# Kernel optimization log

Measured on AMD Instinct MI355X. Metric: run time of the kernel, lower is better.

Reference implementation:

```python
import jax, jax.numpy as jnp
import numpy as np

H, W = 200, 200            # image_size
X_RANGE = (0.0, 100.0)
Y_RANGE = (0.0, 100.0)
SIZE = 36                   # kernel 'size' from source
SIGMA = 3.0
K = SIZE + 1                # kernel is 37x37 (arange(-18, 19))


def _gaussian_kernel():
    r = jnp.arange(-(SIZE // 2), SIZE // 2 + 1, dtype=jnp.float32)
    k1 = jnp.exp(-(r ** 2) / (2.0 * SIGMA ** 2))
    k2 = k1[:, None] * k1[None, :]
    return k2 / k2.sum()    # [K, K]


def setup_inputs() -> dict:
    key = jax.random.key(0)
    # trajectory coords in world units [0, 100) -> spread over whole map
    x_t = jax.random.uniform(key, (512, 64, 2), dtype=jnp.float32) * 100.0
    return {"x_t": x_t}


def reference(x_t):
    B, T, _ = x_t.shape
    x_scale = W / (X_RANGE[1] - X_RANGE[0])
    y_scale = H / (Y_RANGE[1] - Y_RANGE[0])
    # .long() in torch truncates toward zero; inputs are >= 0 here so astype(int32) matches
    x_pix = ((x_t[:, :, 0] - X_RANGE[0]) * x_scale).astype(jnp.int32)   # [B, T]
    y_pix = H - ((x_t[:, :, 1] - Y_RANGE[0]) * y_scale).astype(jnp.int32)
    valid = ~(jnp.isnan(x_t[:, :, 0]) | jnp.isnan(x_t[:, :, 1]))        # [B, T]

    half = SIZE // 2
    x_start = jnp.clip(x_pix - half, 0, W - SIZE)
    y_start = jnp.clip(y_pix - half, 0, H - SIZE)
    x_end = jnp.clip(x_pix + half, 0, W)
    y_end = jnp.clip(y_pix + half, 0, H)
    kx = x_end - x_start    # patch width  (<= 36, kernel[:,:kx] = top-left slice)
    ky = y_end - y_start    # patch height

    kern = _gaussian_kernel()                       # [K, K]
    r = jnp.arange(K)
    c = jnp.arange(K)
    # mask: kernel[:ky, :kx] slice, and point validity            [B, T, K, K]
    mask = ((r[None, None, :, None] < ky[..., None, None])
            & (c[None, None, None, :] < kx[..., None, None])
            & valid[..., None, None])
    vals = jnp.where(mask, kern[None, None, :, :], 0.0)            # [B, T, K, K]
    rows = jnp.clip(y_start[..., None, None] + r[None, None, :, None], 0, H - 1)
    cols = jnp.clip(x_start[..., None, None] + c[None, None, None, :], 0, W - 1)
    rows = jnp.broadcast_to(rows, (B, T, K, K))
    cols = jnp.broadcast_to(cols, (B, T, K, K))
    flat = (rows * W + cols).reshape(B, -1)                        # [B, T*K*K]

    # parallel scatter-add splat of all Gaussian patches
    heat = jnp.zeros((B, H * W), jnp.float32)
    heat = heat.at[jnp.arange(B)[:, None], flat].add(vals.reshape(B, -1))
    heat = heat.reshape(B, H, W)

    # per-image max normalization (max over dim1 then dim2 == max over both)
    m = heat.max(axis=(1, 2), keepdims=True)
    return heat / (m + 1e-10)
```

## Files before the change

### kernel.cpp

```cpp
#include <hip/hip_runtime.h>


#define NT 64
#define TDIM 224
#define BLK 512

typedef short bf16x8 __attribute__((ext_vector_type(8)));
typedef float f32x4  __attribute__((ext_vector_type(4)));

static __device__ inline unsigned short f2bf(float f) {
    unsigned int u = __float_as_uint(f);
    u = (u + 0x7FFFu + ((u >> 16) & 1u)) >> 16;
    return (unsigned short)u;
}

struct __align__(16) SMem {
    unsigned short M[TDIM][64];
    unsigned short stg[8][16][200];
    float k1f[37];
    float wmax[8];
};

__global__ __launch_bounds__(BLK, 4) void heatmap_kernel(const float* __restrict__ x_t,
                                                         float* __restrict__ out) {
    __shared__ SMem s;
    const int tid  = threadIdx.x;
    const int lane = tid & 63;
    const int wv   = tid >> 6;
    const int b    = blockIdx.x;
    const int swl  = (lane & 7) << 4;

    {
        uint4 z = {0u, 0u, 0u, 0u};
        uint4* base = (uint4*)s.M;
        #pragma unroll
        for (int i = 0; i < 4; ++i) {
            const int idx = tid + BLK * i;
            if (idx < 1792) base[idx] = z;
        }
    }
    if (tid < 37) {
        float sum = 0.0f, mine = 0.0f;
        #pragma unroll
        for (int i = 0; i < 37; ++i) {
            float r = (float)(i - 18);
            float v = expf(-(r * r) * (1.0f / 18.0f));
            sum += v;
            if (i == tid) mine = v;
        }
        s.k1f[tid] = mine / sum;
    }
    __syncthreads();

    const int p = tid >> 3, j = tid & 7;
    const float2 xy = *(const float2*)(x_t + (size_t)b * 128 + 2 * p);
    const bool valid = (xy.x == xy.x) && (xy.y == xy.y);
    const int xp = (int)(xy.x * 2.0f);
    const int yp = 200 - (int)(xy.y * 2.0f);
    const int xs = min(max(xp - 18, 0), 164);
    const int ys = min(max(yp - 18, 0), 164);
    const int kx = valid ? (min(max(xp + 18, 0), 200) - xs) : 0;
    const int ky = valid ? (min(max(yp + 18, 0), 200) - ys) : 0;

    #pragma unroll
    for (int i = 0; i < 5; ++i) {
        const int rel = j * 5 + i;
        if (rel < ky) {
            const int row = ys + rel;
            *(unsigned short*)((char*)s.M + row * 128 + ((2 * p) ^ ((row & 7) << 4)))
                = f2bf(s.k1f[rel]);
        }
    }
    __syncthreads();

    const int s1 = wv, s2 = wv + 8;
    bf16x8 A10, A11, A20, A21;
    {
        const char* ab = (const char*)s.M + (16 * s1 + (lane & 15)) * 128;
        A10 = *(const bf16x8*)(ab + ((16 * (lane >> 4)) ^ swl));
        A11 = *(const bf16x8*)(ab + ((16 * (lane >> 4) + 64) ^ swl));
    }
    if (s2 < 13) {
        const char* ab = (const char*)s.M + (16 * s2 + (lane & 15)) * 128;
        A20 = *(const bf16x8*)(ab + ((16 * (lane >> 4)) ^ swl));
        A21 = *(const bf16x8*)(ab + ((16 * (lane >> 4) + 64) ^ swl));
    } else { A20 = A10; A21 = A11; }
    __syncthreads();

    {
        uint4 z = {0u, 0u, 0u, 0u};
        uint4* base = (uint4*)s.M;
        #pragma unroll
        for (int i = 0; i < 4; ++i) {
            const int idx = tid + BLK * i;
            if (idx < 1792) base[idx] = z;
        }
    }
    __syncthreads();
    #pragma unroll
    for (int i = 0; i < 5; ++i) {
        const int rel = j * 5 + i;
        if (rel < kx) {
            const int row = xs + rel;
            *(unsigned short*)((char*)s.M + row * 128 + ((2 * p) ^ ((row & 7) << 4)))
                = f2bf(s.k1f[rel]);
        }
    }
    __syncthreads();

    auto compute_strip = [&](bf16x8 A0, bf16x8 A1, f32x4* acc) {
        #pragma unroll
        for (int t = 0; t < 13; ++t) {
            acc[t][0] = 0.0f; acc[t][1] = 0.0f; acc[t][2] = 0.0f; acc[t][3] = 0.0f;
        }
        #pragma unroll
        for (int t = 0; t < 13; ++t) {
            const char* bb = (const char*)s.M + (16 * t + (lane & 15)) * 128;
            bf16x8 B0 = *(const bf16x8*)(bb + ((16 * (lane >> 4)) ^ swl));
            bf16x8 B1 = *(const bf16x8*)(bb + ((16 * (lane >> 4) + 64) ^ swl));
            acc[t] = __builtin_amdgcn_mfma_f32_16x16x32_bf16(A0, B0, acc[t], 0, 0, 0);
            acc[t] = __builtin_amdgcn_mfma_f32_16x16x32_bf16(A1, B1, acc[t], 0, 0, 0);
        }
    };

    float gmax = 0.0f;
    {
        f32x4 acc[13];
        compute_strip(A10, A11, acc);
        #pragma unroll
        for (int t = 0; t < 13; ++t)
            #pragma unroll
            for (int r = 0; r < 4; ++r) gmax = fmaxf(gmax, acc[t][r]);
        if (s2 < 13) {
            compute_strip(A20, A21, acc);
            #pragma unroll
            for (int t = 0; t < 13; ++t)
                #pragma unroll
                for (int r = 0; r < 4; ++r) gmax = fmaxf(gmax, acc[t][r]);
        }
    }
    #pragma unroll
    for (int off = 32; off > 0; off >>= 1) gmax = fmaxf(gmax, __shfl_xor(gmax, off));
    if (lane == 0) s.wmax[wv] = gmax;
    __syncthreads();
    float mm = s.wmax[0];
    #pragma unroll
    for (int w = 1; w < 8; ++w) mm = fmaxf(mm, s.wmax[w]);
    const float scale = 1.0f / (mm + 1e-10f);

    float* ob = out + (size_t)b * (200 * 200);
    unsigned short* st = &s.stg[wv][0][0];
    auto do_strip = [&](int ss, bf16x8 A0, bf16x8 A1) {
        f32x4 acc[13];
        compute_strip(A0, A1, acc);
        const int r0l = 4 * (lane >> 4), c0l = lane & 15;
        #pragma unroll
        for (int t = 0; t < 13; ++t) {
            const int col = 16 * t + c0l;
            if (col < 200) {
                #pragma unroll
                for (int r = 0; r < 4; ++r)
                    st[(r0l + r) * 200 + col] = f2bf(acc[t][r] * scale);
            }
        }
        __threadfence_block();
        const int nrow = min(16, 200 - 16 * ss);
        float* obs = ob + (size_t)(16 * ss) * 200;
        for (int i = lane; i < nrow * 50; i += 64) {
            uint2 v = *(const uint2*)(st + 4 * i);
            float4 o;
            o.x = __uint_as_float(v.x << 16);
            o.y = __uint_as_float(v.x & 0xFFFF0000u);
            o.z = __uint_as_float(v.y << 16);
            o.w = __uint_as_float(v.y & 0xFFFF0000u);
            *(float4*)(obs + 4 * i) = o;
        }
    };
    do_strip(s1, A10, A11);
    if (s2 < 13) do_strip(s2, A20, A21);
}

extern "C" void kernel_launch(void* const* d_in, const int* in_sizes, int n_in,
                              void* d_out, int out_size, void* d_ws, size_t ws_size,
                              hipStream_t stream) {
    const float* x_t = (const float*)d_in[0];
    float* out = (float*)d_out;
    const int B = in_sizes[0] / (NT * 2);
    heatmap_kernel<<<B, BLK, 0, stream>>>(x_t, out);
}
```

Before: 23.33 us.

## Stage unnormalized MFMA results once and process two images per block

Instead of computing the separable Gaussian outer-product via MFMA twice (once for the max, once for output), each wave stores unnormalized bf16 results into a doubled LDS staging buffer and applies the normalization scale during the global write. Each block now processes two images sequentially, halving the grid, and the occupancy hint in launch bounds is removed. This removes redundant matrix work but increases LDS usage, which reduces blocks per CU, and reduces parallelism across the grid.

```diff
diff --git a/kernel.cpp b/kernel.cpp
--- a/kernel.cpp
+++ b/kernel.cpp
@@ -16,29 +16,19 @@
 
 struct __align__(16) SMem {
     unsigned short M[TDIM][64];
-    unsigned short stg[8][16][200];
+    unsigned short stg[8][2][16][200];
     float k1f[37];
     float wmax[8];
 };
 
-__global__ __launch_bounds__(BLK, 4) void heatmap_kernel(const float* __restrict__ x_t,
-                                                         float* __restrict__ out) {
+__global__ __launch_bounds__(BLK) void heatmap_kernel(const float* __restrict__ x_t,
+                                                      float* __restrict__ out) {
     __shared__ SMem s;
     const int tid  = threadIdx.x;
     const int lane = tid & 63;
     const int wv   = tid >> 6;
-    const int b    = blockIdx.x;
     const int swl  = (lane & 7) << 4;
 
-    {
-        uint4 z = {0u, 0u, 0u, 0u};
-        uint4* base = (uint4*)s.M;
-        #pragma unroll
-        for (int i = 0; i < 4; ++i) {
-            const int idx = tid + BLK * i;
-            if (idx < 1792) base[idx] = z;
-        }
-    }
     if (tid < 37) {
         float sum = 0.0f, mine = 0.0f;
         #pragma unroll
@@ -50,134 +40,138 @@
         }
         s.k1f[tid] = mine / sum;
     }
-    __syncthreads();
-
-    const int p = tid >> 3, j = tid & 7;
-    const float2 xy = *(const float2*)(x_t + (size_t)b * 128 + 2 * p);
-    const bool valid = (xy.x == xy.x) && (xy.y == xy.y);
-    const int xp = (int)(xy.x * 2.0f);
-    const int yp = 200 - (int)(xy.y * 2.0f);
-    const int xs = min(max(xp - 18, 0), 164);
-    const int ys = min(max(yp - 18, 0), 164);
-    const int kx = valid ? (min(max(xp + 18, 0), 200) - xs) : 0;
-    const int ky = valid ? (min(max(yp + 18, 0), 200) - ys) : 0;
-
-    #pragma unroll
-    for (int i = 0; i < 5; ++i) {
-        const int rel = j * 5 + i;
-        if (rel < ky) {
-            const int row = ys + rel;
-            *(unsigned short*)((char*)s.M + row * 128 + ((2 * p) ^ ((row & 7) << 4)))
-                = f2bf(s.k1f[rel]);
-        }
-    }
-    __syncthreads();
 
     const int s1 = wv, s2 = wv + 8;
-    bf16x8 A10, A11, A20, A21;
-    {
-        const char* ab = (const char*)s.M + (16 * s1 + (lane & 15)) * 128;
-        A10 = *(const bf16x8*)(ab + ((16 * (lane >> 4)) ^ swl));
-        A11 = *(const bf16x8*)(ab + ((16 * (lane >> 4) + 64) ^ swl));
-    }
-    if (s2 < 13) {
-        const char* ab = (const char*)s.M + (16 * s2 + (lane & 15)) * 128;
-        A20 = *(const bf16x8*)(ab + ((16 * (lane >> 4)) ^ swl));
-        A21 = *(const bf16x8*)(ab + ((16 * (lane >> 4) + 64) ^ swl));
-    } else { A20 = A10; A21 = A11; }
-    __syncthreads();
 
-    {
-        uint4 z = {0u, 0u, 0u, 0u};
-        uint4* base = (uint4*)s.M;
+    for (int img = 0; img < 2; ++img) {
+        const int b = 2 * blockIdx.x + img;
+
+        __syncthreads();
+        {
+            uint4 z = {0u, 0u, 0u, 0u};
+            uint4* base = (uint4*)s.M;
+            #pragma unroll
+            for (int i = 0; i < 4; ++i) {
+                const int idx = tid + BLK * i;
+                if (idx < 1792) base[idx] = z;
+            }
+        }
+        __syncthreads();
+
+        const int p = tid >> 3, j = tid & 7;
+        const float2 xy = *(const float2*)(x_t + (size_t)b * 128 + 2 * p);
+        const bool valid = (xy.x == xy.x) && (xy.y == xy.y);
+        const int xp = (int)(xy.x * 2.0f);
+        const int yp = 200 - (int)(xy.y * 2.0f);
+        const int xs = min(max(xp - 18, 0), 164);
+        const int ys = min(max(yp - 18, 0), 164);
+        const int kx = valid ? (min(max(xp + 18, 0), 200) - xs) : 0;
+        const int ky = valid ? (min(max(yp + 18, 0), 200) - ys) : 0;
+
         #pragma unroll
-        for (int i = 0; i < 4; ++i) {
-            const int idx = tid + BLK * i;
-            if (idx < 1792) base[idx] = z;
+        for (int i = 0; i < 5; ++i) {
+            const int rel = j * 5 + i;
+            if (rel < ky) {
+                const int row = ys + rel;
+                *(unsigned short*)((char*)s.M + row * 128 + ((2 * p) ^ ((row & 7) << 4)))
+                    = f2bf(s.k1f[rel]);
+            }
         }
-    }
-    __syncthreads();
-    #pragma unroll
-    for (int i = 0; i < 5; ++i) {
-        const int rel = j * 5 + i;
-        if (rel < kx) {
-            const int row = xs + rel;
-            *(unsigned short*)((char*)s.M + row * 128 + ((2 * p) ^ ((row & 7) << 4)))
-                = f2bf(s.k1f[rel]);
+        __syncthreads();
+
+        bf16x8 A10, A11, A20, A21;
+        {
+            const char* ab = (const char*)s.M + (16 * s1 + (lane & 15)) * 128;
+            A10 = *(const bf16x8*)(ab + ((16 * (lane >> 4)) ^ swl));
+            A11 = *(const bf16x8*)(ab + ((16 * (lane >> 4) + 64) ^ swl));
         }
-    }
-    __syncthreads();
+        if (s2 < 13) {
+            const char* ab = (const char*)s.M + (16 * s2 + (lane & 15)) * 128;
+            A20 = *(const bf16x8*)(ab + ((16 * (lane >> 4)) ^ swl));
+            A21 = *(const bf16x8*)(ab + ((16 * (lane >> 4) + 64) ^ swl));
+        } else { A20 = A10; A21 = A11; }
+        __syncthreads();
 
-    auto compute_strip = [&](bf16x8 A0, bf16x8 A1, f32x4* acc) {
+        {
+            uint4 z = {0u, 0u, 0u, 0u};
+            uint4* base = (uint4*)s.M;
+            #pragma unroll
+            for (int i = 0; i < 4; ++i) {
+                const int idx = tid + BLK * i;
+                if (idx < 1792) base[idx] = z;
+            }
+        }
+        __syncthreads();
         #pragma unroll
-        for (int t = 0; t < 13; ++t) {
-            acc[t][0] = 0.0f; acc[t][1] = 0.0f; acc[t][2] = 0.0f; acc[t][3] = 0.0f;
+        for (int i = 0; i < 5; ++i) {
+            const int rel = j * 5 + i;
+            if (rel < kx) {
+                const int row = xs + rel;
+                *(unsigned short*)((char*)s.M + row * 128 + ((2 * p) ^ ((row & 7) << 4)))
+                    = f2bf(s.k1f[rel]);
+            }
         }
-        #pragma unroll
-        for (int t = 0; t < 13; ++t) {
-            const char* bb = (const char*)s.M + (16 * t + (lane & 15)) * 128;
-            bf16x8 B0 = *(const bf16x8*)(bb + ((16 * (lane >> 4)) ^ swl));
-            bf16x8 B1 = *(const bf16x8*)(bb + ((16 * (lane >> 4) + 64) ^ swl));
-            acc[t] = __builtin_amdgcn_mfma_f32_16x16x32_bf16(A0, B0, acc[t], 0, 0, 0);
-            acc[t] = __builtin_amdgcn_mfma_f32_16x16x32_bf16(A1, B1, acc[t], 0, 0, 0);
-        }
-    };
+        __syncthreads();
 
-    float gmax = 0.0f;
-    {
-        f32x4 acc[13];
-        compute_strip(A10, A11, acc);
-        #pragma unroll
-        for (int t = 0; t < 13; ++t)
+        float gmax = 0.0f;
+        const int r0l = 4 * (lane >> 4), c0l = lane & 15;
+        auto compute_stage = [&](int k, bf16x8 A0, bf16x8 A1) {
+            f32x4 acc[13];
             #pragma unroll
-            for (int r = 0; r < 4; ++r) gmax = fmaxf(gmax, acc[t][r]);
-        if (s2 < 13) {
-            compute_strip(A20, A21, acc);
+            for (int t = 0; t < 13; ++t) {
+                acc[t][0] = 0.0f; acc[t][1] = 0.0f; acc[t][2] = 0.0f; acc[t][3] = 0.0f;
+            }
             #pragma unroll
-            for (int t = 0; t < 13; ++t)
+            for (int t = 0; t < 13; ++t) {
+                const char* bb = (const char*)s.M + (16 * t + (lane & 15)) * 128;
+                bf16x8 B0 = *(const bf16x8*)(bb + ((16 * (lane >> 4)) ^ swl));
+                bf16x8 B1 = *(const bf16x8*)(bb + ((16 * (lane >> 4) + 64) ^ swl));
+                acc[t] = __builtin_amdgcn_mfma_f32_16x16x32_bf16(A0, B0, acc[t], 0, 0, 0);
+                acc[t] = __builtin_amdgcn_mfma_f32_16x16x32_bf16(A1, B1, acc[t], 0, 0, 0);
+            }
+            unsigned short* st = &s.stg[wv][k][0][0];
+            #pragma unroll
+            for (int t = 0; t < 13; ++t) {
+                const int col = 16 * t + c0l;
                 #pragma unroll
                 for (int r = 0; r < 4; ++r) gmax = fmaxf(gmax, acc[t][r]);
-        }
+                if (col < 200) {
+                    #pragma unroll
+                    for (int r = 0; r < 4; ++r)
+                        st[(r0l + r) * 200 + col] = f2bf(acc[t][r]);
+                }
+            }
+        };
+        compute_stage(0, A10, A11);
+        if (s2 < 13) compute_stage(1, A20, A21);
+
+        #pragma unroll
+        for (int off = 32; off > 0; off >>= 1) gmax = fmaxf(gmax, __shfl_xor(gmax, off));
+        if (lane == 0) s.wmax[wv] = gmax;
+        __syncthreads();
+        float mm = s.wmax[0];
+        #pragma unroll
+        for (int w = 1; w < 8; ++w) mm = fmaxf(mm, s.wmax[w]);
+        const float scale = 1.0f / (mm + 1e-10f);
+
+        float* ob = out + (size_t)b * (200 * 200);
+        auto drain = [&](int k, int ss) {
+            const unsigned short* st = &s.stg[wv][k][0][0];
+            const int nrow = min(16, 200 - 16 * ss);
+            float* obs = ob + (size_t)(16 * ss) * 200;
+            for (int i = lane; i < nrow * 50; i += 64) {
+                uint2 v = *(const uint2*)(st + 4 * i);
+                float4 o;
+                o.x = __uint_as_float(v.x << 16) * scale;
+                o.y = __uint_as_float(v.x & 0xFFFF0000u) * scale;
+                o.z = __uint_as_float(v.y << 16) * scale;
+                o.w = __uint_as_float(v.y & 0xFFFF0000u) * scale;
+                *(float4*)(obs + 4 * i) = o;
+            }
+        };
+        drain(0, s1);
+        if (s2 < 13) drain(1, s2);
     }
-    #pragma unroll
-    for (int off = 32; off > 0; off >>= 1) gmax = fmaxf(gmax, __shfl_xor(gmax, off));
-    if (lane == 0) s.wmax[wv] = gmax;
-    __syncthreads();
-    float mm = s.wmax[0];
-    #pragma unroll
-    for (int w = 1; w < 8; ++w) mm = fmaxf(mm, s.wmax[w]);
-    const float scale = 1.0f / (mm + 1e-10f);
-
-    float* ob = out + (size_t)b * (200 * 200);
-    unsigned short* st = &s.stg[wv][0][0];
-    auto do_strip = [&](int ss, bf16x8 A0, bf16x8 A1) {
-        f32x4 acc[13];
-        compute_strip(A0, A1, acc);
-        const int r0l = 4 * (lane >> 4), c0l = lane & 15;
-        #pragma unroll
-        for (int t = 0; t < 13; ++t) {
-            const int col = 16 * t + c0l;
-            if (col < 200) {
-                #pragma unroll
-                for (int r = 0; r < 4; ++r)
-                    st[(r0l + r) * 200 + col] = f2bf(acc[t][r] * scale);
-            }
-        }
-        __threadfence_block();
-        const int nrow = min(16, 200 - 16 * ss);
-        float* obs = ob + (size_t)(16 * ss) * 200;
-        for (int i = lane; i < nrow * 50; i += 64) {
-            uint2 v = *(const uint2*)(st + 4 * i);
-            float4 o;
-            o.x = __uint_as_float(v.x << 16);
-            o.y = __uint_as_float(v.x & 0xFFFF0000u);
-            o.z = __uint_as_float(v.y << 16);
-            o.w = __uint_as_float(v.y & 0xFFFF0000u);
-            *(float4*)(obs + 4 * i) = o;
-        }
-    };
-    do_strip(s1, A10, A11);
-    if (s2 < 13) do_strip(s2, A20, A21);
 }
 
 extern "C" void kernel_launch(void* const* d_in, const int* in_sizes, int n_in,
@@ -186,5 +180,5 @@
     const float* x_t = (const float*)d_in[0];
     float* out = (float*)d_out;
     const int B = in_sizes[0] / (NT * 2);
-    heatmap_kernel<<<B, BLK, 0, stream>>>(x_t, out);
+    heatmap_kernel<<<B / 2, BLK, 0, stream>>>(x_t, out);
 }
```

Result: slower. 26.11 us (+11.9%).

## Compute each strip once, stage unscaled bf16, apply max scale on output

Applied to the files above, without the earlier changes.

The kernel used to run the MFMA strip products twice: once to find the per-image max and again to write the normalized output. Now the first strip's products are staged as unscaled bf16 in shared memory and the second strip's accumulators are kept in registers. The normalization scale is applied during the bf16-to-float conversion on store, so the recomputation goes away. In exchange, register pressure rises by 52 floats for acc2, and scaling after bf16 rounding changes rounding slightly. The __threadfence_block between the staging writes and reads was also dropped.

```diff
diff --git a/kernel.cpp b/kernel.cpp
--- a/kernel.cpp
+++ b/kernel.cpp
@@ -108,7 +108,11 @@
     }
     __syncthreads();
 
-    auto compute_strip = [&](bf16x8 A0, bf16x8 A1, f32x4* acc) {
+    const int r0l = 4 * (lane >> 4), c0l = lane & 15;
+    float gmax = 0.0f;
+
+    {
+        f32x4 acc[13];
         #pragma unroll
         for (int t = 0; t < 13; ++t) {
             acc[t][0] = 0.0f; acc[t][1] = 0.0f; acc[t][2] = 0.0f; acc[t][3] = 0.0f;
@@ -118,27 +122,44 @@
             const char* bb = (const char*)s.M + (16 * t + (lane & 15)) * 128;
             bf16x8 B0 = *(const bf16x8*)(bb + ((16 * (lane >> 4)) ^ swl));
             bf16x8 B1 = *(const bf16x8*)(bb + ((16 * (lane >> 4) + 64) ^ swl));
-            acc[t] = __builtin_amdgcn_mfma_f32_16x16x32_bf16(A0, B0, acc[t], 0, 0, 0);
-            acc[t] = __builtin_amdgcn_mfma_f32_16x16x32_bf16(A1, B1, acc[t], 0, 0, 0);
-        }
-    };
-
-    float gmax = 0.0f;
-    {
-        f32x4 acc[13];
-        compute_strip(A10, A11, acc);
-        #pragma unroll
-        for (int t = 0; t < 13; ++t)
+            acc[t] = __builtin_amdgcn_mfma_f32_16x16x32_bf16(A10, B0, acc[t], 0, 0, 0);
+            acc[t] = __builtin_amdgcn_mfma_f32_16x16x32_bf16(A11, B1, acc[t], 0, 0, 0);
+        }
+        unsigned short* st = &s.stg[wv][0][0];
+        #pragma unroll
+        for (int t = 0; t < 13; ++t) {
+            const int col = 16 * t + c0l;
             #pragma unroll
             for (int r = 0; r < 4; ++r) gmax = fmaxf(gmax, acc[t][r]);
-        if (s2 < 13) {
-            compute_strip(A20, A21, acc);
+            if (col < 200) {
+                #pragma unroll
+                for (int r = 0; r < 4; ++r)
+                    st[(r0l + r) * 200 + col] = f2bf(acc[t][r]);
+            }
+        }
+    }
+
+    f32x4 acc2[13];
+    #pragma unroll
+    for (int t = 0; t < 13; ++t) {
+        acc2[t][0] = 0.0f; acc2[t][1] = 0.0f; acc2[t][2] = 0.0f; acc2[t][3] = 0.0f;
+    }
+    if (s2 < 13) {
+        #pragma unroll
+        for (int t = 0; t < 13; ++t) {
+            const char* bb = (const char*)s.M + (16 * t + (lane & 15)) * 128;
+            bf16x8 B0 = *(const bf16x8*)(bb + ((16 * (lane >> 4)) ^ swl));
+            bf16x8 B1 = *(const bf16x8*)(bb + ((16 * (lane >> 4) + 64) ^ swl));
+            acc2[t] = __builtin_amdgcn_mfma_f32_16x16x32_bf16(A20, B0, acc2[t], 0, 0, 0);
+            acc2[t] = __builtin_amdgcn_mfma_f32_16x16x32_bf16(A21, B1, acc2[t], 0, 0, 0);
+        }
+        #pragma unroll
+        for (int t = 0; t < 13; ++t) {
             #pragma unroll
-            for (int t = 0; t < 13; ++t)
-                #pragma unroll
-                for (int r = 0; r < 4; ++r) gmax = fmaxf(gmax, acc[t][r]);
-        }
-    }
+            for (int r = 0; r < 4; ++r) gmax = fmaxf(gmax, acc2[t][r]);
+        }
+    }
+
     #pragma unroll
     for (int off = 32; off > 0; off >>= 1) gmax = fmaxf(gmax, __shfl_xor(gmax, off));
     if (lane == 0) s.wmax[wv] = gmax;
@@ -150,34 +171,41 @@
 
     float* ob = out + (size_t)b * (200 * 200);
     unsigned short* st = &s.stg[wv][0][0];
-    auto do_strip = [&](int ss, bf16x8 A0, bf16x8 A1) {
-        f32x4 acc[13];
-        compute_strip(A0, A1, acc);
-        const int r0l = 4 * (lane >> 4), c0l = lane & 15;
+    {
+        float* obs = ob + (size_t)(16 * s1) * 200;
+        for (int i = lane; i < 16 * 50; i += 64) {
+            uint2 v = *(const uint2*)(st + 4 * i);
+            float4 o;
+            o.x = __uint_as_float(v.x << 16) * scale;
+            o.y = __uint_as_float(v.x & 0xFFFF0000u) * scale;
+            o.z = __uint_as_float(v.y << 16) * scale;
+            o.w = __uint_as_float(v.y & 0xFFFF0000u) * scale;
+            *(float4*)(obs + 4 * i) = o;
+        }
+    }
+
+    if (s2 < 13) {
         #pragma unroll
         for (int t = 0; t < 13; ++t) {
             const int col = 16 * t + c0l;
             if (col < 200) {
                 #pragma unroll
                 for (int r = 0; r < 4; ++r)
-                    st[(r0l + r) * 200 + col] = f2bf(acc[t][r] * scale);
+                    st[(r0l + r) * 200 + col] = f2bf(acc2[t][r]);
             }
         }
-        __threadfence_block();
-        const int nrow = min(16, 200 - 16 * ss);
-        float* obs = ob + (size_t)(16 * ss) * 200;
+        const int nrow = min(16, 200 - 16 * s2);
+        float* obs = ob + (size_t)(16 * s2) * 200;
         for (int i = lane; i < nrow * 50; i += 64) {
             uint2 v = *(const uint2*)(st + 4 * i);
             float4 o;
-            o.x = __uint_as_float(v.x << 16);
-            o.y = __uint_as_float(v.x & 0xFFFF0000u);
-            o.z = __uint_as_float(v.y << 16);
-            o.w = __uint_as_float(v.y & 0xFFFF0000u);
+            o.x = __uint_as_float(v.x << 16) * scale;
+            o.y = __uint_as_float(v.x & 0xFFFF0000u) * scale;
+            o.z = __uint_as_float(v.y << 16) * scale;
+            o.w = __uint_as_float(v.y & 0xFFFF0000u) * scale;
             *(float4*)(obs + 4 * i) = o;
         }
-    };
-    do_strip(s1, A10, A11);
-    if (s2 < 13) do_strip(s2, A20, A21);
+    }
 }
 
 extern "C" void kernel_launch(void* const* d_in, const int* in_sizes, int n_in,
```

Result: slower. 29.09 us (+24.7%).
